# Performance work log

Hardware: AMD Instinct MI355X
Metric: run time of the kernel (lower is better)

Reference implementation:

```python
import jax, jax.numpy as jnp
import numpy as np

# ---- config (matches init_kwargs) ----
ORIGIN_OCC_SHAPE = (16, 200, 200)   # (D_oi, H_oi, W_oi)
INPUT_SIZE = (900, 1600)            # (ih, iw)
DOWN_SAMPLE = 8
GRID_CONFIG = {
    'x_bound': [-40.0, 40.0, 0.4],
    'y_bound': [-40.0, 40.0, 0.4],
    'z_bound': [-1.0, 5.4, 0.4],
    'd_bound': [2.0, 58.0, 1.0],
}


def setup_inputs() -> dict:
    key = jax.random.key(0)
    occ_feature = jax.random.normal(key, (1, 32, 16, 200, 200), dtype=jnp.float32)
    # realistic nuScenes-like intrinsics
    K = jnp.array([[[1266.4, 0.0, 816.3],
                    [0.0, 1266.4, 491.5],
                    [0.0, 0.0, 1.0]]], dtype=jnp.float32)
    # cam->ego: camera looks along ego +x; cam z -> ego x, cam x -> ego -y, cam y -> ego -z
    T = jnp.array([[[0.0, 0.0, 1.0, 1.5],
                    [-1.0, 0.0, 0.0, 0.0],
                    [0.0, -1.0, 0.0, 1.5],
                    [0.0, 0.0, 0.0, 1.0]]], dtype=jnp.float32)
    return {'occ_feature': occ_feature, 'K': K, 'T': T}


def get_sampling_points():
    ih, iw = INPUT_SIZE
    fh, fw = ih // DOWN_SAMPLE, iw // DOWN_SAMPLE
    d0, d1, dstep = GRID_CONFIG['d_bound']
    fd = int((d1 - d0) // dstep)
    x = jnp.linspace(0.0, iw - 1.0, fw)
    y = jnp.linspace(0.0, ih - 1.0, fh)
    d = jnp.linspace(d0, d1, fd)
    gd, gy, gx = jnp.meshgrid(d, y, x, indexing='ij')   # (fd, fh, fw)
    # homogeneous image points scaled by depth: [x*d, y*d, d, 1]
    pts = jnp.stack([gx * gd, gy * gd, gd, jnp.ones_like(gd)], axis=-1)
    return pts  # (fd, fh, fw, 4)


def grid_sample_3d(vol, grid):
    """Trilinear grid_sample, padding_mode='zeros', align_corners=True.
    vol: (B,C,D,H,W); grid: (B,Do,Ho,Wo,3) with (x,y,z) in [-1,1] -> (W,H,D)."""
    B, C, D, H, W = vol.shape
    gx, gy, gz = grid[..., 0], grid[..., 1], grid[..., 2]
    x = (gx + 1.0) * 0.5 * (W - 1)
    y = (gy + 1.0) * 0.5 * (H - 1)
    z = (gz + 1.0) * 0.5 * (D - 1)
    x0 = jnp.floor(x); y0 = jnp.floor(y); z0 = jnp.floor(z)
    tx = x - x0; ty = y - y0; tz = z - z0
    vol_flat = vol.reshape(B, C, D * H * W)

    def corner(zc, yc, xc, w):
        valid = (xc >= 0) & (xc <= W - 1) & (yc >= 0) & (yc <= H - 1) & (zc >= 0) & (zc <= D - 1)
        zi = jnp.clip(zc, 0, D - 1).astype(jnp.int32)
        yi = jnp.clip(yc, 0, H - 1).astype(jnp.int32)
        xi = jnp.clip(xc, 0, W - 1).astype(jnp.int32)
        idx = ((zi * H + yi) * W + xi).reshape(B, 1, -1)          # (B,1,M)
        g = jnp.take_along_axis(vol_flat, idx, axis=2)            # (B,C,M)
        wm = jnp.where(valid, w, 0.0).reshape(B, 1, -1)
        return g * wm

    out = (corner(z0, y0, x0, (1 - tz) * (1 - ty) * (1 - tx))
           + corner(z0, y0, x0 + 1, (1 - tz) * (1 - ty) * tx)
           + corner(z0, y0 + 1, x0, (1 - tz) * ty * (1 - tx))
           + corner(z0, y0 + 1, x0 + 1, (1 - tz) * ty * tx)
           + corner(z0 + 1, y0, x0, tz * (1 - ty) * (1 - tx))
           + corner(z0 + 1, y0, x0 + 1, tz * (1 - ty) * tx)
           + corner(z0 + 1, y0 + 1, x0, tz * ty * (1 - tx))
           + corner(z0 + 1, y0 + 1, x0 + 1, tz * ty * tx))
    Do, Ho, Wo = grid.shape[1:4]
    return out.reshape(B, C, Do, Ho, Wo)


def volume_transform(occ_feature, K, T):
    B, C, D_occ, H_occ, W_occ = occ_feature.shape
    D_oi, H_oi, W_oi = ORIGIN_OCC_SHAPE
    ratio = (W_oi / W_occ, H_oi / H_occ, D_oi / D_occ)
    xb, yb, zb = GRID_CONFIG['x_bound'], GRID_CONFIG['y_bound'], GRID_CONFIG['z_bound']

    # ego -> ego-feature-grid affine (4x4)
    e2f = jnp.eye(4, dtype=jnp.float32)
    e2f = e2f.at[0, 0].set(1.0 / xb[2] / ratio[0])
    e2f = e2f.at[1, 1].set(1.0 / yb[2] / ratio[1])
    e2f = e2f.at[2, 2].set(1.0 / zb[2] / ratio[2])
    e2f = e2f.at[0, 3].set(-xb[0] / xb[2] / ratio[0])
    e2f = e2f.at[1, 3].set(-yb[0] / yb[2] / ratio[1])
    e2f = e2f.at[2, 3].set(-zb[0] / zb[2] / ratio[2])

    # cam2img 4x4 with K in top-left, then invert (matches torch.inverse path)
    cam2img = jnp.tile(jnp.eye(4, dtype=K.dtype)[None], (B, 1, 1))
    cam2img = cam2img.at[:, :3, :3].set(K)
    img2cam = jnp.linalg.inv(cam2img)                  # (B,4,4)

    # fused projection matrix: ego2egofeat @ T @ img2cam
    M = jnp.einsum('ij,bjk,bkl->bil', e2f, T, img2cam)  # (B,4,4)

    pts = get_sampling_points()                         # (fd,fh,fw,4)
    feat_pts = jnp.einsum('bij,dhwj->bdhwi', M, pts)[..., :3]  # (B,fd,fh,fw,3)

    norm = jnp.array([W_occ - 1, H_occ - 1, D_occ - 1], dtype=jnp.float32)
    grid = feat_pts / norm * 2.0 - 1.0

    sampled = grid_sample_3d(occ_feature, grid)         # (B,C,fd,fh,fw)
    return jnp.sum(sampled, axis=2)                     # (B,C,fh,fw)


def reference(occ_feature, K, T):
    return volume_transform(occ_feature, K, T)
```

## Files before the change

kernel.cpp:

```cpp
#include <hip/hip_runtime.h>

#define FD 56
#define FH 112
#define FW 200
#define VD 16
#define VH 200
#define VW 200
#define NC 32
#define NPIX (FH * FW)
#define NS   (VD * VH * VW)
#define CSTRIDE NS

typedef float f2v __attribute__((ext_vector_type(2)));
typedef f2v uf2v4 __attribute__((aligned(4)));
typedef _Float16 h4 __attribute__((ext_vector_type(4)));
typedef h4 uh4 __attribute__((aligned(8)));
typedef _Float16 h8 __attribute__((ext_vector_type(8)));

__device__ inline void compute_M(const float* Km, const float* Tm, float* M) {
    float a = Km[0], b = Km[1], c = Km[2];
    float d = Km[3], e = Km[4], f = Km[5];
    float g = Km[6], h = Km[7], i = Km[8];
    float A00 = e * i - f * h, A01 = c * h - b * i, A02 = b * f - c * e;
    float A10 = f * g - d * i, A11 = a * i - c * g, A12 = c * d - a * f;
    float A20 = d * h - e * g, A21 = b * g - a * h, A22 = a * e - b * d;
    float det = a * A00 + b * A10 + c * A20;
    float r = 1.0f / det;
    float Ki[9] = {A00 * r, A01 * r, A02 * r,
                   A10 * r, A11 * r, A12 * r,
                   A20 * r, A21 * r, A22 * r};
    float R[4][4];
    for (int rr = 0; rr < 4; ++rr) {
        for (int cc = 0; cc < 3; ++cc)
            R[rr][cc] = Tm[rr * 4 + 0] * Ki[0 * 3 + cc]
                      + Tm[rr * 4 + 1] * Ki[1 * 3 + cc]
                      + Tm[rr * 4 + 2] * Ki[2 * 3 + cc];
        R[rr][3] = Tm[rr * 4 + 3];
    }
    const float s[3] = {2.5f, 2.5f, 2.5f};
    const float t[3] = {100.0f, 100.0f, 2.5f};
    for (int rr = 0; rr < 3; ++rr)
        for (int cc = 0; cc < 4; ++cc)
            M[rr * 4 + cc] = s[rr] * R[rr][cc] + t[rr] * R[3][cc];
}

__global__ __launch_bounds__(256)
void vt_transpose_h(const float* __restrict__ vol, _Float16* __restrict__ volT,
                    const float* __restrict__ Km, const float* __restrict__ Tm) {
    __shared__ float tile[256 * 33];
    __shared__ int s_skip;
    const int t  = threadIdx.x;
    const int s0 = blockIdx.x * 256;

    if (t == 0) {
        float M[12];
        compute_M(Km, Tm, M);
        const float b00 = M[0], b01 = M[1], b02 = M[2],  tx3 = M[3];
        const float b10 = M[4], b11 = M[5], b12 = M[6],  ty3 = M[7];
        const float b20 = M[8], b21 = M[9], b22 = M[10], tz3 = M[11];
        const float C00 = b11 * b22 - b12 * b21;
        const float C01 = b02 * b21 - b01 * b22;
        const float C02 = b01 * b12 - b02 * b11;
        const float C10 = b12 * b20 - b10 * b22;
        const float C11 = b00 * b22 - b02 * b20;
        const float C12 = b02 * b10 - b00 * b12;
        const float C20 = b10 * b21 - b11 * b20;
        const float C21 = b01 * b20 - b00 * b21;
        const float C22 = b00 * b11 - b01 * b10;
        const float det = b00 * C00 + b01 * C10 + b02 * C20;
        int skip = 0;
        if (fabsf(det) > 1e-12f) {
            const float r = 1.0f / det;
            const float ix0 = C00 * r, ix1 = C01 * r, ix2 = C02 * r;
            const float iy0 = C10 * r, iy1 = C11 * r, iy2 = C12 * r;
            const float iz0 = C20 * r, iz1 = C21 * r, iz2 = C22 * r;
            const float cx = -(ix0 * tx3 + ix1 * ty3 + ix2 * tz3);
            const float cy = -(iy0 * tx3 + iy1 * ty3 + iy2 * tz3);
            const float cz = -(iz0 * tx3 + iz1 * ty3 + iz2 * tz3);
            const int send = s0 + 255;
            const int z0 = s0 / (VH * VW), z1 = send / (VH * VW);
            float ylo = 0.0f, yhi = (float)(VH - 1);
            if (z0 == z1) {
                const int r0 = s0 - z0 * (VH * VW);
                ylo = (float)(r0 / VW);
                yhi = (float)((r0 + 255) / VW);
            }
            const float EXP = 1.25f;
            const float lo[3] = {0.0f - EXP, ylo - EXP, (float)z0 - EXP};
            const float hi[3] = {(float)(VW - 1) + EXP, yhi + EXP, (float)z1 + EXP};
            const float SLK = 10.0f;
            const float gc[6][3] = {
                { iz0,  iz1,  iz2},
                {-iz0, -iz1, -iz2},
                { ix0,  ix1,  ix2},
                {1599.f*iz0 - ix0, 1599.f*iz1 - ix1, 1599.f*iz2 - ix2},
                { iy0,  iy1,  iy2},
                { 899.f*iz0 - iy0,  899.f*iz1 - iy1,  899.f*iz2 - iy2},
            };
            const float gd0[6] = {cz - 2.0f + 0.1f, 58.0f + 0.1f - cz,
                                  cx + SLK, 1599.f * cz - cx + SLK,
                                  cy + SLK,  899.f * cz - cy + SLK};
            for (int q = 0; q < 6; ++q) {
                float m = gd0[q];
                for (int j = 0; j < 3; ++j)
                    m += (gc[q][j] > 0.0f) ? gc[q][j] * hi[j] : gc[q][j] * lo[j];
                if (m < 0.0f) { skip = 1; break; }
            }
        }
        s_skip = skip;
    }
    __syncthreads();
    if (s_skip) return;

#pragma unroll
    for (int c = 0; c < NC; ++c)
        tile[t * 33 + c] = __builtin_nontemporal_load(vol + (size_t)c * CSTRIDE + s0 + t);
    __syncthreads();
    const int rs  = t >> 2;
    const int ch8 = (t & 3) * 8;
#pragma unroll
    for (int j = 0; j < 4; ++j) {
        const int sl = j * 64 + rs;
        const float* r = &tile[sl * 33 + ch8];
        h8 pk = {(_Float16)r[0], (_Float16)r[1], (_Float16)r[2], (_Float16)r[3],
                 (_Float16)r[4], (_Float16)r[5], (_Float16)r[6], (_Float16)r[7]};
        *(h8*)(volT + (size_t)(s0 + sl) * NC + ch8) = pk;
    }
}

__global__ __launch_bounds__(256)
void vt_sample_th(const _Float16* __restrict__ volT,
                  const float* __restrict__ Km,
                  const float* __restrict__ Tm,
                  float* __restrict__ out) {
    __shared__ float sM[12];
    if (threadIdx.x == 0) compute_M(Km, Tm, sM);
    __syncthreads();

    const int t    = threadIdx.x;
    const int wv   = t >> 6;
    const int lane = t & 63;
    const int chq  = lane & 7;
    const int pixl = lane >> 3;
    const int c0   = chq * 4;
    const int p    = blockIdx.x * 32 + wv * 8 + pixl;
    const int py   = p / FW;
    const int px   = p - py * FW;

    const float gx = (float)px * (1599.0f / 199.0f);
    const float gy = (float)py * (899.0f / 111.0f);

    const float m03 = sM[3], m13 = sM[7], m23 = sM[11];
    const float ax = sM[0] * gx + sM[1] * gy + sM[2];
    const float ay = sM[4] * gx + sM[5] * gy + sM[6];
    const float az = sM[8] * gx + sM[9] * gy + sM[10];

    float dlo = 2.0f, dhi = 58.0f;
    {
        const float A[3]  = {ax, ay, az};
        const float Bv[3] = {m03, m13, m23};
        const float HI[3] = {(float)VW, (float)VH, (float)VD};
        for (int q = 0; q < 3; ++q) {
            float a = A[q], b = Bv[q], hi = HI[q];
            if (a > 0.0f)      { dlo = fmaxf(dlo, (-1.0f - b) / a); dhi = fminf(dhi, (hi - b) / a); }
            else if (a < 0.0f) { dlo = fmaxf(dlo, (hi - b) / a);    dhi = fminf(dhi, (-1.0f - b) / a); }
            else if (!(b > -1.0f && b < hi)) { dlo = 1e30f; dhi = -1e30f; }
        }
    }
    int klo = (int)ceilf((dlo - 2.0f) * (55.0f / 56.0f));
    int khi = (int)floorf((dhi - 2.0f) * (55.0f / 56.0f));
    klo = max(klo - 1, 0);
    khi = min(khi + 1, FD - 1);

    float acc0 = 0.0f, acc1 = 0.0f, acc2 = 0.0f, acc3 = 0.0f;

#pragma unroll 2
    for (int k = klo; k <= khi; ++k) {
        const float gd = 2.0f + (float)k * (56.0f / 55.0f);
        const float fx = fmaf(ax, gd, m03);
        const float fy = fmaf(ay, gd, m13);
        const float fz = fmaf(az, gd, m23);

        const bool valid = (fx > -1.0f) && (fx < (float)VW) &&
                           (fy > -1.0f) && (fy < (float)VH) &&
                           (fz > -1.0f) && (fz < (float)VD);
        const float vm = valid ? 1.0f : 0.0f;

        const float xf = floorf(fx), yf = floorf(fy), zf = floorf(fz);
        const float tx = fx - xf, ty = fy - yf, tz = fz - zf;
        const int ix = (int)xf, iy = (int)yf, iz = (int)zf;

        const float wx0 = (ix >= 0)     ? (1.0f - tx) : 0.0f;
        const float wx1 = (ix < VW - 1) ? tx          : 0.0f;
        const float wy0 = (iy >= 0)     ? (1.0f - ty) : 0.0f;
        const float wy1 = (iy < VH - 1) ? ty          : 0.0f;
        const float wz0 = ((iz >= 0)     ? (1.0f - tz) : 0.0f) * vm;
        const float wz1 = ((iz < VD - 1) ? tz          : 0.0f) * vm;

        const int xi0 = min(max(ix,     0), VW - 1);
        const int xi1 = min(max(ix + 1, 0), VW - 1);
        const int yo0 = min(max(iy,     0), VH - 1) * VW;
        const int yo1 = min(max(iy + 1, 0), VH - 1) * VW;
        const int zo0 = min(max(iz,     0), VD - 1) * (VH * VW);
        const int zo1 = min(max(iz + 1, 0), VD - 1) * (VH * VW);

        const int o000 = ((zo0 + yo0 + xi0) << 5) + c0;
        const int o001 = ((zo0 + yo0 + xi1) << 5) + c0;
        const int o010 = ((zo0 + yo1 + xi0) << 5) + c0;
        const int o011 = ((zo0 + yo1 + xi1) << 5) + c0;
        const int o100 = ((zo1 + yo0 + xi0) << 5) + c0;
        const int o101 = ((zo1 + yo0 + xi1) << 5) + c0;
        const int o110 = ((zo1 + yo1 + xi0) << 5) + c0;
        const int o111 = ((zo1 + yo1 + xi1) << 5) + c0;

        const h4 v000 = *(const uh4*)(volT + o000);
        const h4 v001 = *(const uh4*)(volT + o001);
        const h4 v010 = *(const uh4*)(volT + o010);
        const h4 v011 = *(const uh4*)(volT + o011);
        const h4 v100 = *(const uh4*)(volT + o100);
        const h4 v101 = *(const uh4*)(volT + o101);
        const h4 v110 = *(const uh4*)(volT + o110);
        const h4 v111 = *(const uh4*)(volT + o111);

        const float w000 = wz0 * wy0 * wx0, w001 = wz0 * wy0 * wx1;
        const float w010 = wz0 * wy1 * wx0, w011 = wz0 * wy1 * wx1;
        const float w100 = wz1 * wy0 * wx0, w101 = wz1 * wy0 * wx1;
        const float w110 = wz1 * wy1 * wx0, w111 = wz1 * wy1 * wx1;

        acc0 += w000 * (float)v000.x + w001 * (float)v001.x
              + w010 * (float)v010.x + w011 * (float)v011.x
              + w100 * (float)v100.x + w101 * (float)v101.x
              + w110 * (float)v110.x + w111 * (float)v111.x;
        acc1 += w000 * (float)v000.y + w001 * (float)v001.y
              + w010 * (float)v010.y + w011 * (float)v011.y
              + w100 * (float)v100.y + w101 * (float)v101.y
              + w110 * (float)v110.y + w111 * (float)v111.y;
        acc2 += w000 * (float)v000.z + w001 * (float)v001.z
              + w010 * (float)v010.z + w011 * (float)v011.z
              + w100 * (float)v100.z + w101 * (float)v101.z
              + w110 * (float)v110.z + w111 * (float)v111.z;
        acc3 += w000 * (float)v000.w + w001 * (float)v001.w
              + w010 * (float)v010.w + w011 * (float)v011.w
              + w100 * (float)v100.w + w101 * (float)v101.w
              + w110 * (float)v110.w + w111 * (float)v111.w;
    }

    out[(size_t)(c0 + 0) * NPIX + p] = acc0;
    out[(size_t)(c0 + 1) * NPIX + p] = acc1;
    out[(size_t)(c0 + 2) * NPIX + p] = acc2;
    out[(size_t)(c0 + 3) * NPIX + p] = acc3;
}

__global__ __launch_bounds__(256)
void vt_sample_direct(const float* __restrict__ vol,
                      const float* __restrict__ Km,
                      const float* __restrict__ Tm,
                      float* __restrict__ out) {
    __shared__ float sM[12];
    if (threadIdx.x == 0) compute_M(Km, Tm, sM);
    __syncthreads();

    const int cg   = blockIdx.x & 3;
    const int pg   = blockIdx.x >> 2;
    const int lane = threadIdx.x & 63;
    const int wv   = threadIdx.x >> 6;
    const int c0   = (cg * 4 + wv) * 2;
    const int p    = pg * 64 + lane;
    const int py   = p / FW;
    const int px   = p - py * FW;

    const float gx = (float)px * (1599.0f / 199.0f);
    const float gy = (float)py * (899.0f / 111.0f);

    const float m03 = sM[3], m13 = sM[7], m23 = sM[11];
    const float ax = sM[0] * gx + sM[1] * gy + sM[2];
    const float ay = sM[4] * gx + sM[5] * gy + sM[6];
    const float az = sM[8] * gx + sM[9] * gy + sM[10];

    float dlo = 2.0f, dhi = 58.0f;
    {
        const float A[3]  = {ax, ay, az};
        const float Bv[3] = {m03, m13, m23};
        const float HI[3] = {(float)VW, (float)VH, (float)VD};
        for (int q = 0; q < 3; ++q) {
            float a = A[q], b = Bv[q], hi = HI[q];
            if (a > 0.0f)      { dlo = fmaxf(dlo, (-1.0f - b) / a); dhi = fminf(dhi, (hi - b) / a); }
            else if (a < 0.0f) { dlo = fmaxf(dlo, (hi - b) / a);    dhi = fminf(dhi, (-1.0f - b) / a); }
            else if (!(b > -1.0f && b < hi)) { dlo = 1e30f; dhi = -1e30f; }
        }
    }
    int klo = (int)ceilf((dlo - 2.0f) * (55.0f / 56.0f));
    int khi = (int)floorf((dhi - 2.0f) * (55.0f / 56.0f));
    klo = max(klo - 1, 0);
    khi = min(khi + 1, FD - 1);

    const float* __restrict__ volc0 = vol + (size_t)c0 * CSTRIDE;
    const float* __restrict__ volc1 = volc0 + CSTRIDE;
    float acc0 = 0.0f, acc1 = 0.0f;

#pragma unroll 2
    for (int k = klo; k <= khi; ++k) {
        const float gd = 2.0f + (float)k * (56.0f / 55.0f);
        const float fx = fmaf(ax, gd, m03);
        const float fy = fmaf(ay, gd, m13);
        const float fz = fmaf(az, gd, m23);

        const bool valid = (fx > -1.0f) && (fx < (float)VW) &&
                           (fy > -1.0f) && (fy < (float)VH) &&
                           (fz > -1.0f) && (fz < (float)VD);
        const float vm = valid ? 1.0f : 0.0f;

        const float xf = floorf(fx), yf = floorf(fy), zf = floorf(fz);
        const float tx = fx - xf, ty = fy - yf, tz = fz - zf;
        const int ix = (int)xf, iy = (int)yf, iz = (int)zf;

        float wlo = (ix >= 0) ? (1.0f - tx) : tx;
        wlo = (ix >= VW - 1) ? 0.0f : wlo;
        float whi = (ix >= 0) ? tx : 0.0f;
        whi = (ix >= VW - 1) ? (1.0f - tx) : whi;

        const float wy0 = (iy >= 0)     ? (1.0f - ty) : 0.0f;
        const float wy1 = (iy < VH - 1) ? ty          : 0.0f;
        const float wz0 = ((iz >= 0)     ? (1.0f - tz) : 0.0f) * vm;
        const float wz1 = ((iz < VD - 1) ? tz          : 0.0f) * vm;
        const float w00 = wz0 * wy0, w01 = wz0 * wy1;
        const float w10 = wz1 * wy0, w11 = wz1 * wy1;

        const int xi0 = min(max(ix, 0), VW - 2);
        const int yo0 = min(max(iy,     0), VH - 1) * VW;
        const int yo1 = min(max(iy + 1, 0), VH - 1) * VW;
        const int zo0 = min(max(iz,     0), VD - 1) * (VH * VW);
        const int zo1 = min(max(iz + 1, 0), VD - 1) * (VH * VW);

        const int o00 = zo0 + yo0 + xi0, o01 = zo0 + yo1 + xi0;
        const int o10 = zo1 + yo0 + xi0, o11 = zo1 + yo1 + xi0;

        const f2v a00 = *(const uf2v4*)(volc0 + o00);
        const f2v a01 = *(const uf2v4*)(volc0 + o01);
        const f2v a10 = *(const uf2v4*)(volc0 + o10);
        const f2v a11 = *(const uf2v4*)(volc0 + o11);
        const f2v b00 = *(const uf2v4*)(volc1 + o00);
        const f2v b01 = *(const uf2v4*)(volc1 + o01);
        const f2v b10 = *(const uf2v4*)(volc1 + o10);
        const f2v b11 = *(const uf2v4*)(volc1 + o11);

        acc0 += w00 * (wlo * a00.x + whi * a00.y) + w01 * (wlo * a01.x + whi * a01.y)
              + w10 * (wlo * a10.x + whi * a10.y) + w11 * (wlo * a11.x + whi * a11.y);
        acc1 += w00 * (wlo * b00.x + whi * b00.y) + w01 * (wlo * b01.x + whi * b01.y)
              + w10 * (wlo * b10.x + whi * b10.y) + w11 * (wlo * b11.x + whi * b11.y);
    }

    out[c0 * NPIX + p]       = acc0;
    out[(c0 + 1) * NPIX + p] = acc1;
}

extern "C" void kernel_launch(void* const* d_in, const int* in_sizes, int n_in,
                              void* d_out, int out_size, void* d_ws, size_t ws_size,
                              hipStream_t stream) {
    (void)in_sizes; (void)n_in; (void)out_size;
    const float* vol = (const float*)d_in[0];
    const float* Km  = (const float*)d_in[1];
    const float* Tm  = (const float*)d_in[2];
    float* out = (float*)d_out;

    const size_t need = (size_t)NS * NC * sizeof(_Float16);
    if (ws_size >= need) {
        _Float16* volT = (_Float16*)d_ws;
        vt_transpose_h<<<dim3(NS / 256), dim3(256), 0, stream>>>(vol, volT, Km, Tm);
        vt_sample_th<<<dim3(NPIX / 32), dim3(256), 0, stream>>>(volT, Km, Tm, out);
    } else {
        vt_sample_direct<<<dim3(1400), dim3(256), 0, stream>>>(vol, Km, Tm, out);
    }
}
```

Baseline: 145.7 us.

## Tile transpose kernel in 3D blocks for tighter frustum culling and drop LDS staging

The transpose/convert kernel now launches over 3D tiles of 32x8 voxels per z-slice instead of linear 256-voxel runs. The frustum test runs on a compact x/y/z box, so more blocks outside the camera view can skip their loads and stores. The shared-memory staging is also removed: each thread loads its 32 channels into registers and writes 64 contiguous bytes. In exchange, reads are only 32 floats wide per row, about 12% of lanes sit idle in the partial last x tile, and the per-thread 64-byte stores are less coalesced.

```diff
diff --git a/kernel.cpp b/kernel.cpp
--- a/kernel.cpp
+++ b/kernel.cpp
@@ -10,6 +10,9 @@
 #define NPIX (FH * FW)
 #define NS   (VD * VH * VW)
 #define CSTRIDE NS
+
+#define TXW 32
+#define TYH 8
 
 typedef float f2v __attribute__((ext_vector_type(2)));
 typedef f2v uf2v4 __attribute__((aligned(4)));
@@ -47,10 +50,11 @@
 __global__ __launch_bounds__(256)
 void vt_transpose_h(const float* __restrict__ vol, _Float16* __restrict__ volT,
                     const float* __restrict__ Km, const float* __restrict__ Tm) {
-    __shared__ float tile[256 * 33];
     __shared__ int s_skip;
     const int t  = threadIdx.x;
-    const int s0 = blockIdx.x * 256;
+    const int x0 = blockIdx.x * TXW;
+    const int y0 = blockIdx.y * TYH;
+    const int z  = blockIdx.z;
 
     if (t == 0) {
         float M[12];
@@ -77,17 +81,10 @@
             const float cx = -(ix0 * tx3 + ix1 * ty3 + ix2 * tz3);
             const float cy = -(iy0 * tx3 + iy1 * ty3 + iy2 * tz3);
             const float cz = -(iz0 * tx3 + iz1 * ty3 + iz2 * tz3);
-            const int send = s0 + 255;
-            const int z0 = s0 / (VH * VW), z1 = send / (VH * VW);
-            float ylo = 0.0f, yhi = (float)(VH - 1);
-            if (z0 == z1) {
-                const int r0 = s0 - z0 * (VH * VW);
-                ylo = (float)(r0 / VW);
-                yhi = (float)((r0 + 255) / VW);
-            }
             const float EXP = 1.25f;
-            const float lo[3] = {0.0f - EXP, ylo - EXP, (float)z0 - EXP};
-            const float hi[3] = {(float)(VW - 1) + EXP, yhi + EXP, (float)z1 + EXP};
+            const float lo[3] = {(float)x0 - EXP, (float)y0 - EXP, (float)z - EXP};
+            const float hi[3] = {(float)min(x0 + TXW - 1, VW - 1) + EXP,
+                                 (float)(y0 + TYH - 1) + EXP, (float)z + EXP};
             const float SLK = 10.0f;
             const float gc[6][3] = {
                 { iz0,  iz1,  iz2},
@@ -112,19 +109,24 @@
     __syncthreads();
     if (s_skip) return;
 
+    const int lx = t & (TXW - 1);
+    const int ly = t >> 5;
+    const int x  = x0 + lx;
+    if (x >= VW) return;
+    const int s = (z * VH + (y0 + ly)) * VW + x;
+
+    float v[NC];
 #pragma unroll
     for (int c = 0; c < NC; ++c)
-        tile[t * 33 + c] = __builtin_nontemporal_load(vol + (size_t)c * CSTRIDE + s0 + t);
-    __syncthreads();
-    const int rs  = t >> 2;
-    const int ch8 = (t & 3) * 8;
+        v[c] = __builtin_nontemporal_load(vol + (size_t)c * CSTRIDE + s);
+
+    _Float16* dst = volT + (size_t)s * NC;
 #pragma unroll
     for (int j = 0; j < 4; ++j) {
-        const int sl = j * 64 + rs;
-        const float* r = &tile[sl * 33 + ch8];
+        const float* r = &v[j * 8];
         h8 pk = {(_Float16)r[0], (_Float16)r[1], (_Float16)r[2], (_Float16)r[3],
                  (_Float16)r[4], (_Float16)r[5], (_Float16)r[6], (_Float16)r[7]};
-        *(h8*)(volT + (size_t)(s0 + sl) * NC + ch8) = pk;
+        *(h8*)(dst + j * 8) = pk;
     }
 }
 
@@ -366,7 +368,7 @@
     const size_t need = (size_t)NS * NC * sizeof(_Float16);
     if (ws_size >= need) {
         _Float16* volT = (_Float16*)d_ws;
-        vt_transpose_h<<<dim3(NS / 256), dim3(256), 0, stream>>>(vol, volT, Km, Tm);
+        vt_transpose_h<<<dim3(7, VH / TYH, VD), dim3(256), 0, stream>>>(vol, volT, Km, Tm);
         vt_sample_th<<<dim3(NPIX / 32), dim3(256), 0, stream>>>(volT, Km, Tm, out);
     } else {
         vt_sample_direct<<<dim3(1400), dim3(256), 0, stream>>>(vol, Km, Tm, out);
```

After: 146.3 us. About the same (+0.5%).
